# Performance work log

Measured on AMD Instinct MI355X. Metric: run time of the kernel, lower is better.

The kernel has to match this reference:

```python
import jax, jax.numpy as jnp
import numpy as np

B, T, H, N, IN, W, D = 4096, 128, 64, 16, 32, 128, 8


def lipswish(x):
    return 0.909 * jax.nn.silu(x)


def setup_inputs() -> dict:
    key = jax.random.key(0)
    ks = jax.random.split(key, 10)

    def lin(k, i, o):
        kw, kb = jax.random.split(k)
        w = jax.random.normal(kw, (i, o), jnp.float32) / np.sqrt(i).astype(np.float32)
        b = jax.random.normal(kb, (o,), jnp.float32) * 0.01
        return w, b

    init_w0, init_b0 = lin(ks[0], IN, W)
    init_w1, init_b1 = lin(ks[1], W, H)
    drift_w0, drift_b0 = lin(ks[2], H + 1, W)
    drift_w1, drift_b1 = lin(ks[3], W, H)
    diff_w0, diff_b0 = lin(ks[4], H + 1, W)
    diff_w1, diff_b1 = lin(ks[5], W, H * N)
    ro_w, ro_b = lin(ks[6], H, D)
    ts = jnp.arange(T, dtype=jnp.float32)
    init_noise = jax.random.normal(ks[7], (B, IN), jnp.float32)
    # Brownian increments for unit steps: dW ~ N(0, dt) with dt = 1.
    dW = jax.random.normal(ks[8], (B, T - 1, N), jnp.float32)
    return dict(ts=ts, init_noise=init_noise, dW=dW,
                init_w0=init_w0, init_b0=init_b0, init_w1=init_w1, init_b1=init_b1,
                drift_w0=drift_w0, drift_b0=drift_b0, drift_w1=drift_w1, drift_b1=drift_b1,
                diff_w0=diff_w0, diff_b0=diff_b0, diff_w1=diff_w1, diff_b1=diff_b1,
                ro_w=ro_w, ro_b=ro_b)


def reference(ts, init_noise, dW,
              init_w0, init_b0, init_w1, init_b1,
              drift_w0, drift_b0, drift_w1, drift_b1,
              diff_w0, diff_b0, diff_w1, diff_b1,
              ro_w, ro_b):
    # initial MLP: default relu activation, identity final activation
    y0 = jnp.maximum(init_noise @ init_w0 + init_b0, 0.0) @ init_w1 + init_b1  # [B, H]

    def with_t(t, y):
        return jnp.concatenate([jnp.full((y.shape[0], 1), t, y.dtype), y], axis=1)

    def drift(t, y):  # [B, H]
        h = lipswish(with_t(t, y) @ drift_w0 + drift_b0)
        return jnp.tanh(h @ drift_w1 + drift_b1)

    def diffusion(t, y):  # [B, H, N]
        h = lipswish(with_t(t, y) @ diff_w0 + diff_b0)
        g = jnp.tanh(h @ diff_w1 + diff_b1)
        return g.reshape(y.shape[0], H, N)

    f0 = drift(ts[0], y0)
    g0 = diffusion(ts[0], y0)

    def step(carry, inp):
        y, yhat, f, g = carry
        t0, t1, dw = inp  # dw: [B, N]
        dt = t1 - t0
        # ReversibleHeun: yhat1 = 2 y - yhat + (f dt + g dW)
        yhat1 = 2.0 * y - yhat + f * dt + jnp.einsum('bhn,bn->bh', g, dw)
        f1 = drift(t1, yhat1)
        g1 = diffusion(t1, yhat1)
        y1 = y + 0.5 * ((f + f1) * dt + jnp.einsum('bhn,bn->bh', g + g1, dw))
        return (y1, yhat1, f1, g1), y1

    dWs = jnp.swapaxes(dW, 0, 1)  # [T-1, B, N]
    _, ys = jax.lax.scan(step, (y0, y0, f0, g0), (ts[:-1], ts[1:], dWs))
    ys = jnp.concatenate([y0[None], ys], axis=0)  # [T, B, H]
    out = jnp.einsum('tbh,hd->tbd', ys, ro_w) + ro_b
    return jnp.swapaxes(out, 0, 1)  # [B, T, D]
```

## Files before the change

### kernel.cpp

```cpp
#include <hip/hip_runtime.h>

#define NTHREADS 512
#define BB 8
#define SP 68
#define SH 132


struct alignas(16) SMem {
    float dw0[65 * 128];
    float gw0[65 * 128];
    float db0[128];
    float db1[64];
    float gb0[128];
    float ro[512];
    float rob[8];
    float y[BB * SP];
    float yh[BB * SP];
    float f[BB * SP];
    float h[BB * SH];
    float dwn[BB * 16];
};

__device__ __forceinline__ float lipswish_f(float x) {
    const float e = expf(-x);
    const float d = __fadd_rn(1.0f, e);
    const float t = __fmul_rn(0.909f, x);
    return __fdiv_rn(t, d);
}

__global__ __launch_bounds__(NTHREADS, 4)
void sde_kernel(const float* __restrict__ ts, const float* __restrict__ init_noise,
                const float* __restrict__ dWin,
                const float* __restrict__ iw0, const float* __restrict__ ib0,
                const float* __restrict__ iw1, const float* __restrict__ ib1,
                const float* __restrict__ dr_w0, const float* __restrict__ dr_b0,
                const float* __restrict__ dr_w1, const float* __restrict__ dr_b1,
                const float* __restrict__ di_w0, const float* __restrict__ di_b0,
                const float* __restrict__ di_w1, const float* __restrict__ di_b1,
                const float* __restrict__ ro_w, const float* __restrict__ ro_b,
                float* __restrict__ out)
{
    __shared__ SMem sm;
    const int tid  = threadIdx.x;
    const int lane = tid & 63;
    const int wv   = tid >> 6;
    const int b0   = blockIdx.x * BB;

    const int r    = lane & 1;
    const int qn   = (lane >> 1) & 3;
    const int a    = lane >> 3;
    const int c0   = wv * 128 + (lane >> 1) * 4;
    const int rb0  = r * 4;
    const int hh_own = wv * 8 + a;
    const bool owner = ((lane & 6) == 0);
    const int fb = lane >> 3;
    const int fc = wv * 8 + (lane & 7);

    for (int i = tid; i < 65 * 128; i += NTHREADS) {
        sm.dw0[i] = dr_w0[i];
        sm.gw0[i] = di_w0[i];
    }
    if (tid < 128) sm.db0[tid] = dr_b0[tid];
    if (tid < 64)  sm.db1[tid] = dr_b1[tid];
    if (tid < 128) sm.gb0[tid] = di_b0[tid];
    if (tid < 512) sm.ro[tid] = ro_w[tid];
    if (tid < 8) sm.rob[tid] = ro_b[tid];

    float gb1v[4];
    {
        const float4 bv = *(const float4*)&di_b1[c0];
        gb1v[0] = bv.x; gb1v[1] = bv.y; gb1v[2] = bv.z; gb1v[3] = bv.w;
    }

    for (int i = tid; i < BB * 32; i += NTHREADS)
        sm.f[i] = init_noise[(size_t)(b0 + (i >> 5)) * 32 + (i & 31)];
    __syncthreads();

    {
        const int j = tid & 127, bq = tid >> 7;
        float acc[2];
        const float bj = ib0[j];
#pragma unroll
        for (int bi = 0; bi < 2; ++bi) acc[bi] = bj;
        for (int i = 0; i < 32; ++i) {
            const float w = iw0[i * 128 + j];
#pragma unroll
            for (int bi = 0; bi < 2; ++bi)
                acc[bi] = __fmaf_rn(sm.f[(bq * 2 + bi) * 32 + i], w, acc[bi]);
        }
#pragma unroll
        for (int bi = 0; bi < 2; ++bi)
            sm.h[(bq * 2 + bi) * SH + j] = fmaxf(acc[bi], 0.0f);
    }
    __syncthreads();
    {
        const int hh = tid & 63, bg = tid >> 6;
        float acc = ib1[hh];
        for (int k = 0; k < 128; ++k)
            acc = __fmaf_rn(sm.h[bg * SH + k], iw1[k * 64 + hh], acc);
        sm.y[bg * SP + hh]  = acc;
        sm.yh[bg * SP + hh] = acc;
    }
    __syncthreads();

    auto readout = [&](int trow) {
        if (tid < 64) {
            const int b = tid >> 3, d = tid & 7;
            float acc = sm.rob[d];
#pragma unroll
            for (int hh = 0; hh < 64; ++hh)
                acc = __fmaf_rn(sm.y[b * SP + hh], sm.ro[hh * 8 + d], acc);
            out[((size_t)(b0 + b) * 128 + trow) * 8 + d] = acc;
        }
    };
    readout(0);

    float g[4][4];

    auto layer1 = [&](const float* w0s, const float* b0s, float t1f) {
        const int j = tid & 127, bq = tid >> 7;
        float acc[2];
        const float bj = b0s[j];
        const float wt = w0s[j];
#pragma unroll
        for (int bi = 0; bi < 2; ++bi) acc[bi] = __fmaf_rn(t1f, wt, bj);
#pragma unroll 4
        for (int i = 0; i < 64; i += 4) {
            const float w0_ = w0s[(1 + i) * 128 + j];
            const float w1_ = w0s[(2 + i) * 128 + j];
            const float w2_ = w0s[(3 + i) * 128 + j];
            const float w3_ = w0s[(4 + i) * 128 + j];
#pragma unroll
            for (int bi = 0; bi < 2; ++bi) {
                const float4 xv = *(const float4*)&sm.yh[(bq * 2 + bi) * SP + i];
                acc[bi] = __fmaf_rn(xv.x, w0_, acc[bi]);
                acc[bi] = __fmaf_rn(xv.y, w1_, acc[bi]);
                acc[bi] = __fmaf_rn(xv.z, w2_, acc[bi]);
                acc[bi] = __fmaf_rn(xv.w, w3_, acc[bi]);
            }
        }
#pragma unroll
        for (int bi = 0; bi < 2; ++bi)
            sm.h[(bq * 2 + bi) * SH + j] = lipswish_f(acc[bi]);
    };

    auto ein_bfly = [&](const float v[4], int b) -> float {
        float part = 0.0f;
#pragma unroll
        for (int e = 0; e < 4; ++e)
            part = __fmaf_rn(v[e], sm.dwn[b * 16 + qn * 4 + e], part);
        part = __fadd_rn(part, __shfl_xor(part, 2, 64));
        part = __fadd_rn(part, __shfl_xor(part, 4, 64));
        return part;
    };

    auto mlp = [&](float t1f, float dtf, bool upd) {
        layer1(sm.dw0, sm.db0, t1f);
        __syncthreads();
        {
            float acc = sm.db1[fc];
#pragma unroll 4
            for (int k = 0; k < 128; ++k)
                acc = __fmaf_rn(sm.h[fb * SH + k], dr_w1[k * 64 + fc], acc);
            sm.f[fb * SP + fc] = tanhf(acc);
        }
        __syncthreads();
        layer1(sm.gw0, sm.gb0, t1f);
        __syncthreads();
        {
            float acc[4][4];
#pragma unroll
            for (int bi = 0; bi < 4; ++bi)
#pragma unroll
                for (int e = 0; e < 4; ++e) acc[bi][e] = 0.0f;

            float4 wA[4], wB[4], hA[4], hB[4];
#pragma unroll
            for (int t = 0; t < 4; ++t)
                wA[t] = *(const float4*)&di_w1[(size_t)t * 1024 + c0];
#pragma unroll
            for (int bi = 0; bi < 4; ++bi)
                hA[bi] = *(const float4*)&sm.h[(rb0 + bi) * SH];

#pragma unroll 1
            for (int kb = 0; kb < 128; kb += 8) {
                const int k2 = kb + 4;
#pragma unroll
                for (int t = 0; t < 4; ++t)
                    wB[t] = *(const float4*)&di_w1[(size_t)(k2 + t) * 1024 + c0];
#pragma unroll
                for (int bi = 0; bi < 4; ++bi)
                    hB[bi] = *(const float4*)&sm.h[(rb0 + bi) * SH + k2];
#pragma unroll
                for (int bi = 0; bi < 4; ++bi) {
                    acc[bi][0] = __fmaf_rn(hA[bi].x, wA[0].x, acc[bi][0]);
                    acc[bi][1] = __fmaf_rn(hA[bi].x, wA[0].y, acc[bi][1]);
                    acc[bi][2] = __fmaf_rn(hA[bi].x, wA[0].z, acc[bi][2]);
                    acc[bi][3] = __fmaf_rn(hA[bi].x, wA[0].w, acc[bi][3]);
                    acc[bi][0] = __fmaf_rn(hA[bi].y, wA[1].x, acc[bi][0]);
                    acc[bi][1] = __fmaf_rn(hA[bi].y, wA[1].y, acc[bi][1]);
                    acc[bi][2] = __fmaf_rn(hA[bi].y, wA[1].z, acc[bi][2]);
                    acc[bi][3] = __fmaf_rn(hA[bi].y, wA[1].w, acc[bi][3]);
                    acc[bi][0] = __fmaf_rn(hA[bi].z, wA[2].x, acc[bi][0]);
                    acc[bi][1] = __fmaf_rn(hA[bi].z, wA[2].y, acc[bi][1]);
                    acc[bi][2] = __fmaf_rn(hA[bi].z, wA[2].z, acc[bi][2]);
                    acc[bi][3] = __fmaf_rn(hA[bi].z, wA[2].w, acc[bi][3]);
                    acc[bi][0] = __fmaf_rn(hA[bi].w, wA[3].x, acc[bi][0]);
                    acc[bi][1] = __fmaf_rn(hA[bi].w, wA[3].y, acc[bi][1]);
                    acc[bi][2] = __fmaf_rn(hA[bi].w, wA[3].z, acc[bi][2]);
                    acc[bi][3] = __fmaf_rn(hA[bi].w, wA[3].w, acc[bi][3]);
                }
                const int k3 = (kb + 8) & 127;
#pragma unroll
                for (int t = 0; t < 4; ++t)
                    wA[t] = *(const float4*)&di_w1[(size_t)(k3 + t) * 1024 + c0];
#pragma unroll
                for (int bi = 0; bi < 4; ++bi)
                    hA[bi] = *(const float4*)&sm.h[(rb0 + bi) * SH + k3];
#pragma unroll
                for (int bi = 0; bi < 4; ++bi) {
                    acc[bi][0] = __fmaf_rn(hB[bi].x, wB[0].x, acc[bi][0]);
                    acc[bi][1] = __fmaf_rn(hB[bi].x, wB[0].y, acc[bi][1]);
                    acc[bi][2] = __fmaf_rn(hB[bi].x, wB[0].z, acc[bi][2]);
                    acc[bi][3] = __fmaf_rn(hB[bi].x, wB[0].w, acc[bi][3]);
                    acc[bi][0] = __fmaf_rn(hB[bi].y, wB[1].x, acc[bi][0]);
                    acc[bi][1] = __fmaf_rn(hB[bi].y, wB[1].y, acc[bi][1]);
                    acc[bi][2] = __fmaf_rn(hB[bi].y, wB[1].z, acc[bi][2]);
                    acc[bi][3] = __fmaf_rn(hB[bi].y, wB[1].w, acc[bi][3]);
                    acc[bi][0] = __fmaf_rn(hB[bi].z, wB[2].x, acc[bi][0]);
                    acc[bi][1] = __fmaf_rn(hB[bi].z, wB[2].y, acc[bi][1]);
                    acc[bi][2] = __fmaf_rn(hB[bi].z, wB[2].z, acc[bi][2]);
                    acc[bi][3] = __fmaf_rn(hB[bi].z, wB[2].w, acc[bi][3]);
                    acc[bi][0] = __fmaf_rn(hB[bi].w, wB[3].x, acc[bi][0]);
                    acc[bi][1] = __fmaf_rn(hB[bi].w, wB[3].y, acc[bi][1]);
                    acc[bi][2] = __fmaf_rn(hB[bi].w, wB[3].z, acc[bi][2]);
                    acc[bi][3] = __fmaf_rn(hB[bi].w, wB[3].w, acc[bi][3]);
                }
            }

#pragma unroll
            for (int bi = 0; bi < 4; ++bi) {
                const int b = rb0 + bi;
                float gv4[4];
#pragma unroll
                for (int e = 0; e < 4; ++e) {
                    const float gv = tanhf(__fadd_rn(acc[bi][e], gb1v[e]));
                    gv4[e] = gv;
                    g[bi][e] = gv;
                }
                if (upd) {
                    const float ein2 = ein_bfly(gv4, b);
                    if (owner) {
                        const int idx = b * SP + hh_own;
                        const float tot = __fmaf_rn(dtf, sm.f[idx], ein2);
                        sm.y[idx] = __fmaf_rn(0.5f, tot, sm.y[idx]);
                    }
                }
            }
        }
        __syncthreads();
    };

    mlp(ts[0], 0.0f, false);

    for (int s = 0; s < 127; ++s) {
        const float t1f = ts[s + 1];
        const float dtf = __fsub_rn(t1f, ts[s]);

        if (tid < BB * 16)
            sm.dwn[tid] = dWin[((size_t)(b0 + (tid >> 4)) * 127 + s) * 16 + (tid & 15)];
        __syncthreads();

#pragma unroll
        for (int bi = 0; bi < 4; ++bi) {
            const int b = rb0 + bi;
            const float ein1 = ein_bfly(g[bi], b);
            if (owner) {
                const int idx = b * SP + hh_own;
                const float yv  = sm.y[idx];
                const float yhv = sm.yh[idx];
                const float inc = __fmaf_rn(dtf, sm.f[idx], ein1);
                const float a1  = __fmaf_rn(2.0f, yv, -yhv);
                sm.yh[idx] = __fadd_rn(a1, inc);
                sm.y[idx]  = __fmaf_rn(0.5f, inc, yv);
            }
        }
        __syncthreads();

        mlp(t1f, dtf, true);
        readout(s + 1);
    }
}

extern "C" void kernel_launch(void* const* d_in, const int* in_sizes, int n_in,
                              void* d_out, int out_size, void* d_ws, size_t ws_size,
                              hipStream_t stream) {
    (void)in_sizes; (void)n_in; (void)d_ws; (void)ws_size; (void)out_size;
    const float* ts         = (const float*)d_in[0];
    const float* init_noise = (const float*)d_in[1];
    const float* dW         = (const float*)d_in[2];
    const float* iw0        = (const float*)d_in[3];
    const float* ib0        = (const float*)d_in[4];
    const float* iw1        = (const float*)d_in[5];
    const float* ib1        = (const float*)d_in[6];
    const float* dr_w0      = (const float*)d_in[7];
    const float* dr_b0      = (const float*)d_in[8];
    const float* dr_w1      = (const float*)d_in[9];
    const float* dr_b1      = (const float*)d_in[10];
    const float* di_w0      = (const float*)d_in[11];
    const float* di_b0      = (const float*)d_in[12];
    const float* di_w1      = (const float*)d_in[13];
    const float* di_b1      = (const float*)d_in[14];
    const float* ro_w       = (const float*)d_in[15];
    const float* ro_b       = (const float*)d_in[16];
    float* out = (float*)d_out;

    sde_kernel<<<dim3(4096 / BB), dim3(NTHREADS), 0, stream>>>(
        ts, init_noise, dW, iw0, ib0, iw1, ib1,
        dr_w0, dr_b0, dr_w1, dr_b1, di_w0, di_b0, di_w1, di_b1,
        ro_w, ro_b, out);
}
```

Baseline: 3.762 ms.

## Double block threads, drop LDS weight copies, remap diffusion GEMM thread tiling

Raises the block to 1024 threads and remaps the diffusion output-layer work so each thread computes 2 batch rows by 4 columns instead of 4 by 4. The einsum butterfly reduction is changed to match the new lane layout. The first-layer weights for drift and diffusion are now read straight from global memory instead of being staged in LDS, which shrinks shared memory and is meant to allow more resident blocks and higher occupancy. The trade-off is repeated global/L2 reads of those weights at every step, plus half the threads idling in some phases.

Result: slower. 6.048 ms (+60.8%).

```diff
diff --git a/kernel.cpp b/kernel.cpp
--- a/kernel.cpp
+++ b/kernel.cpp
@@ -1,14 +1,12 @@
 #include <hip/hip_runtime.h>
 
-#define NTHREADS 512
+#define NTHREADS 1024
 #define BB 8
 #define SP 68
 #define SH 132
 
 
 struct alignas(16) SMem {
-    float dw0[65 * 128];
-    float gw0[65 * 128];
     float db0[128];
     float db1[64];
     float gb0[128];
@@ -28,7 +26,7 @@
     return __fdiv_rn(t, d);
 }
 
-__global__ __launch_bounds__(NTHREADS, 4)
+__global__ __launch_bounds__(NTHREADS, 8)
 void sde_kernel(const float* __restrict__ ts, const float* __restrict__ init_noise,
                 const float* __restrict__ dWin,
                 const float* __restrict__ iw0, const float* __restrict__ ib0,
@@ -46,20 +44,18 @@
     const int wv   = tid >> 6;
     const int b0   = blockIdx.x * BB;
 
-    const int r    = lane & 1;
-    const int qn   = (lane >> 1) & 3;
-    const int a    = lane >> 3;
-    const int c0   = wv * 128 + (lane >> 1) * 4;
-    const int rb0  = r * 4;
-    const int hh_own = wv * 8 + a;
-    const bool owner = ((lane & 6) == 0);
+    const int cg   = wv & 3;
+    const int rr   = wv >> 2;
+    const int rb0  = rr * 2;
+    const int c0   = cg * 256 + (lane << 2);
+    const int qn   = lane & 3;
+    const int hh_own = cg * 16 + (lane >> 2);
+    const bool owner = (qn == 0);
     const int fb = lane >> 3;
-    const int fc = wv * 8 + (lane & 7);
-
-    for (int i = tid; i < 65 * 128; i += NTHREADS) {
-        sm.dw0[i] = dr_w0[i];
-        sm.gw0[i] = di_w0[i];
-    }
+    const int fc = (wv & 7) * 8 + (lane & 7);
+    const int l1j = tid & 127;
+    const int l1b = tid >> 7;
+
     if (tid < 128) sm.db0[tid] = dr_b0[tid];
     if (tid < 64)  sm.db1[tid] = dr_b1[tid];
     if (tid < 128) sm.gb0[tid] = di_b0[tid];
@@ -72,28 +68,18 @@
         gb1v[0] = bv.x; gb1v[1] = bv.y; gb1v[2] = bv.z; gb1v[3] = bv.w;
     }
 
-    for (int i = tid; i < BB * 32; i += NTHREADS)
-        sm.f[i] = init_noise[(size_t)(b0 + (i >> 5)) * 32 + (i & 31)];
+    if (tid < BB * 32)
+        sm.f[tid] = init_noise[(size_t)(b0 + (tid >> 5)) * 32 + (tid & 31)];
     __syncthreads();
 
     {
-        const int j = tid & 127, bq = tid >> 7;
-        float acc[2];
-        const float bj = ib0[j];
-#pragma unroll
-        for (int bi = 0; bi < 2; ++bi) acc[bi] = bj;
-        for (int i = 0; i < 32; ++i) {
-            const float w = iw0[i * 128 + j];
-#pragma unroll
-            for (int bi = 0; bi < 2; ++bi)
-                acc[bi] = __fmaf_rn(sm.f[(bq * 2 + bi) * 32 + i], w, acc[bi]);
-        }
-#pragma unroll
-        for (int bi = 0; bi < 2; ++bi)
-            sm.h[(bq * 2 + bi) * SH + j] = fmaxf(acc[bi], 0.0f);
+        float acc = ib0[l1j];
+        for (int i = 0; i < 32; ++i)
+            acc = __fmaf_rn(sm.f[l1b * 32 + i], iw0[i * 128 + l1j], acc);
+        sm.h[l1b * SH + l1j] = fmaxf(acc, 0.0f);
     }
     __syncthreads();
-    {
+    if (tid < 512) {
         const int hh = tid & 63, bg = tid >> 6;
         float acc = ib1[hh];
         for (int k = 0; k < 128; ++k)
@@ -115,33 +101,24 @@
     };
     readout(0);
 
-    float g[4][4];
-
-    auto layer1 = [&](const float* w0s, const float* b0s, float t1f) {
-        const int j = tid & 127, bq = tid >> 7;
-        float acc[2];
-        const float bj = b0s[j];
-        const float wt = w0s[j];
-#pragma unroll
-        for (int bi = 0; bi < 2; ++bi) acc[bi] = __fmaf_rn(t1f, wt, bj);
+    float g[2][4];
+
+    auto layer1 = [&](const float* __restrict__ w0g, const float* __restrict__ b0l,
+                      float t1f) {
+        float acc = __fmaf_rn(t1f, w0g[l1j], b0l[l1j]);
 #pragma unroll 4
         for (int i = 0; i < 64; i += 4) {
-            const float w0_ = w0s[(1 + i) * 128 + j];
-            const float w1_ = w0s[(2 + i) * 128 + j];
-            const float w2_ = w0s[(3 + i) * 128 + j];
-            const float w3_ = w0s[(4 + i) * 128 + j];
-#pragma unroll
-            for (int bi = 0; bi < 2; ++bi) {
-                const float4 xv = *(const float4*)&sm.yh[(bq * 2 + bi) * SP + i];
-                acc[bi] = __fmaf_rn(xv.x, w0_, acc[bi]);
-                acc[bi] = __fmaf_rn(xv.y, w1_, acc[bi]);
-                acc[bi] = __fmaf_rn(xv.z, w2_, acc[bi]);
-                acc[bi] = __fmaf_rn(xv.w, w3_, acc[bi]);
-            }
-        }
-#pragma unroll
-        for (int bi = 0; bi < 2; ++bi)
-            sm.h[(bq * 2 + bi) * SH + j] = lipswish_f(acc[bi]);
+            const float w0_ = w0g[(1 + i) * 128 + l1j];
+            const float w1_ = w0g[(2 + i) * 128 + l1j];
+            const float w2_ = w0g[(3 + i) * 128 + l1j];
+            const float w3_ = w0g[(4 + i) * 128 + l1j];
+            const float4 xv = *(const float4*)&sm.yh[l1b * SP + i];
+            acc = __fmaf_rn(xv.x, w0_, acc);
+            acc = __fmaf_rn(xv.y, w1_, acc);
+            acc = __fmaf_rn(xv.z, w2_, acc);
+            acc = __fmaf_rn(xv.w, w3_, acc);
+        }
+        sm.h[l1b * SH + l1j] = lipswish_f(acc);
     };
 
     auto ein_bfly = [&](const float v[4], int b) -> float {
@@ -149,15 +126,15 @@
 #pragma unroll
         for (int e = 0; e < 4; ++e)
             part = __fmaf_rn(v[e], sm.dwn[b * 16 + qn * 4 + e], part);
+        part = __fadd_rn(part, __shfl_xor(part, 1, 64));
         part = __fadd_rn(part, __shfl_xor(part, 2, 64));
-        part = __fadd_rn(part, __shfl_xor(part, 4, 64));
         return part;
     };
 
     auto mlp = [&](float t1f, float dtf, bool upd) {
-        layer1(sm.dw0, sm.db0, t1f);
-        __syncthreads();
-        {
+        layer1(dr_w0, sm.db0, t1f);
+        __syncthreads();
+        if (tid < 512) {
             float acc = sm.db1[fc];
 #pragma unroll 4
             for (int k = 0; k < 128; ++k)
@@ -165,81 +142,45 @@
             sm.f[fb * SP + fc] = tanhf(acc);
         }
         __syncthreads();
-        layer1(sm.gw0, sm.gb0, t1f);
+        layer1(di_w0, sm.gb0, t1f);
         __syncthreads();
         {
-            float acc[4][4];
-#pragma unroll
-            for (int bi = 0; bi < 4; ++bi)
+            float acc[2][4];
+#pragma unroll
+            for (int bi = 0; bi < 2; ++bi)
 #pragma unroll
                 for (int e = 0; e < 4; ++e) acc[bi][e] = 0.0f;
 
-            float4 wA[4], wB[4], hA[4], hB[4];
-#pragma unroll
-            for (int t = 0; t < 4; ++t)
-                wA[t] = *(const float4*)&di_w1[(size_t)t * 1024 + c0];
-#pragma unroll
-            for (int bi = 0; bi < 4; ++bi)
-                hA[bi] = *(const float4*)&sm.h[(rb0 + bi) * SH];
-
-#pragma unroll 1
-            for (int kb = 0; kb < 128; kb += 8) {
-                const int k2 = kb + 4;
-#pragma unroll
-                for (int t = 0; t < 4; ++t)
-                    wB[t] = *(const float4*)&di_w1[(size_t)(k2 + t) * 1024 + c0];
-#pragma unroll
-                for (int bi = 0; bi < 4; ++bi)
-                    hB[bi] = *(const float4*)&sm.h[(rb0 + bi) * SH + k2];
-#pragma unroll
-                for (int bi = 0; bi < 4; ++bi) {
-                    acc[bi][0] = __fmaf_rn(hA[bi].x, wA[0].x, acc[bi][0]);
-                    acc[bi][1] = __fmaf_rn(hA[bi].x, wA[0].y, acc[bi][1]);
-                    acc[bi][2] = __fmaf_rn(hA[bi].x, wA[0].z, acc[bi][2]);
-                    acc[bi][3] = __fmaf_rn(hA[bi].x, wA[0].w, acc[bi][3]);
-                    acc[bi][0] = __fmaf_rn(hA[bi].y, wA[1].x, acc[bi][0]);
-                    acc[bi][1] = __fmaf_rn(hA[bi].y, wA[1].y, acc[bi][1]);
-                    acc[bi][2] = __fmaf_rn(hA[bi].y, wA[1].z, acc[bi][2]);
-                    acc[bi][3] = __fmaf_rn(hA[bi].y, wA[1].w, acc[bi][3]);
-                    acc[bi][0] = __fmaf_rn(hA[bi].z, wA[2].x, acc[bi][0]);
-                    acc[bi][1] = __fmaf_rn(hA[bi].z, wA[2].y, acc[bi][1]);
-                    acc[bi][2] = __fmaf_rn(hA[bi].z, wA[2].z, acc[bi][2]);
-                    acc[bi][3] = __fmaf_rn(hA[bi].z, wA[2].w, acc[bi][3]);
-                    acc[bi][0] = __fmaf_rn(hA[bi].w, wA[3].x, acc[bi][0]);
-                    acc[bi][1] = __fmaf_rn(hA[bi].w, wA[3].y, acc[bi][1]);
-                    acc[bi][2] = __fmaf_rn(hA[bi].w, wA[3].z, acc[bi][2]);
-                    acc[bi][3] = __fmaf_rn(hA[bi].w, wA[3].w, acc[bi][3]);
-                }
-                const int k3 = (kb + 8) & 127;
-#pragma unroll
-                for (int t = 0; t < 4; ++t)
-                    wA[t] = *(const float4*)&di_w1[(size_t)(k3 + t) * 1024 + c0];
-#pragma unroll
-                for (int bi = 0; bi < 4; ++bi)
-                    hA[bi] = *(const float4*)&sm.h[(rb0 + bi) * SH + k3];
-#pragma unroll
-                for (int bi = 0; bi < 4; ++bi) {
-                    acc[bi][0] = __fmaf_rn(hB[bi].x, wB[0].x, acc[bi][0]);
-                    acc[bi][1] = __fmaf_rn(hB[bi].x, wB[0].y, acc[bi][1]);
-                    acc[bi][2] = __fmaf_rn(hB[bi].x, wB[0].z, acc[bi][2]);
-                    acc[bi][3] = __fmaf_rn(hB[bi].x, wB[0].w, acc[bi][3]);
-                    acc[bi][0] = __fmaf_rn(hB[bi].y, wB[1].x, acc[bi][0]);
-                    acc[bi][1] = __fmaf_rn(hB[bi].y, wB[1].y, acc[bi][1]);
-                    acc[bi][2] = __fmaf_rn(hB[bi].y, wB[1].z, acc[bi][2]);
-                    acc[bi][3] = __fmaf_rn(hB[bi].y, wB[1].w, acc[bi][3]);
-                    acc[bi][0] = __fmaf_rn(hB[bi].z, wB[2].x, acc[bi][0]);
-                    acc[bi][1] = __fmaf_rn(hB[bi].z, wB[2].y, acc[bi][1]);
-                    acc[bi][2] = __fmaf_rn(hB[bi].z, wB[2].z, acc[bi][2]);
-                    acc[bi][3] = __fmaf_rn(hB[bi].z, wB[2].w, acc[bi][3]);
-                    acc[bi][0] = __fmaf_rn(hB[bi].w, wB[3].x, acc[bi][0]);
-                    acc[bi][1] = __fmaf_rn(hB[bi].w, wB[3].y, acc[bi][1]);
-                    acc[bi][2] = __fmaf_rn(hB[bi].w, wB[3].z, acc[bi][2]);
-                    acc[bi][3] = __fmaf_rn(hB[bi].w, wB[3].w, acc[bi][3]);
+#pragma unroll 2
+            for (int kb = 0; kb < 128; kb += 4) {
+                const float4 w0 = *(const float4*)&di_w1[(size_t)(kb + 0) * 1024 + c0];
+                const float4 w1 = *(const float4*)&di_w1[(size_t)(kb + 1) * 1024 + c0];
+                const float4 w2 = *(const float4*)&di_w1[(size_t)(kb + 2) * 1024 + c0];
+                const float4 w3 = *(const float4*)&di_w1[(size_t)(kb + 3) * 1024 + c0];
+#pragma unroll
+                for (int bi = 0; bi < 2; ++bi) {
+                    const float4 hv = *(const float4*)&sm.h[(rb0 + bi) * SH + kb];
+                    acc[bi][0] = __fmaf_rn(hv.x, w0.x, acc[bi][0]);
+                    acc[bi][1] = __fmaf_rn(hv.x, w0.y, acc[bi][1]);
+                    acc[bi][2] = __fmaf_rn(hv.x, w0.z, acc[bi][2]);
+                    acc[bi][3] = __fmaf_rn(hv.x, w0.w, acc[bi][3]);
+                    acc[bi][0] = __fmaf_rn(hv.y, w1.x, acc[bi][0]);
+                    acc[bi][1] = __fmaf_rn(hv.y, w1.y, acc[bi][1]);
+                    acc[bi][2] = __fmaf_rn(hv.y, w1.z, acc[bi][2]);
+                    acc[bi][3] = __fmaf_rn(hv.y, w1.w, acc[bi][3]);
+                    acc[bi][0] = __fmaf_rn(hv.z, w2.x, acc[bi][0]);
+                    acc[bi][1] = __fmaf_rn(hv.z, w2.y, acc[bi][1]);
+                    acc[bi][2] = __fmaf_rn(hv.z, w2.z, acc[bi][2]);
+                    acc[bi][3] = __fmaf_rn(hv.z, w2.w, acc[bi][3]);
+                    acc[bi][0] = __fmaf_rn(hv.w, w3.x, acc[bi][0]);
+                    acc[bi][1] = __fmaf_rn(hv.w, w3.y, acc[bi][1]);
+                    acc[bi][2] = __fmaf_rn(hv.w, w3.z, acc[bi][2]);
+                    acc[bi][3] = __fmaf_rn(hv.w, w3.w, acc[bi][3]);
                 }
             }
 
 #pragma unroll
-            for (int bi = 0; bi < 4; ++bi) {
+            for (int bi = 0; bi < 2; ++bi) {
                 const int b = rb0 + bi;
                 float gv4[4];
 #pragma unroll
@@ -272,7 +213,7 @@
         __syncthreads();
 
 #pragma unroll
-        for (int bi = 0; bi < 4; ++bi) {
+        for (int bi = 0; bi < 2; ++bi) {
             const int b = rb0 + bi;
             const float ein1 = ein_bfly(g[bi], b);
             if (owner) {
```

## Halve block to 4 batch rows and read first-layer weights from global

Applied to the files above, without the earlier changes.

Reduces the block from 512 threads and 8 batch rows to 256 threads and 4 rows, and remaps the diffusion second-layer ownership so each thread covers all 4 rows with a 2-step butterfly reduction. It also drops the two 65x128 first-layer weight tables from LDS, reading them straight from global memory (L1/L2 cached). The aim is to shrink shared memory per block so more blocks fit per CU and the serial step chain overlaps better. In exchange, global weight traffic per batch row doubles and the per-block setup staging is gone.

Result: slower. 4.271 ms (+13.5%).

```diff
diff --git a/kernel.cpp b/kernel.cpp
--- a/kernel.cpp
+++ b/kernel.cpp
@@ -1,14 +1,12 @@
 #include <hip/hip_runtime.h>
 
-#define NTHREADS 512
-#define BB 8
+#define NTHREADS 256
+#define BB 4
 #define SP 68
 #define SH 132
 
 
 struct alignas(16) SMem {
-    float dw0[65 * 128];
-    float gw0[65 * 128];
     float db0[128];
     float db1[64];
     float gb0[128];
@@ -46,24 +44,17 @@
     const int wv   = tid >> 6;
     const int b0   = blockIdx.x * BB;
 
-    const int r    = lane & 1;
-    const int qn   = (lane >> 1) & 3;
-    const int a    = lane >> 3;
-    const int c0   = wv * 128 + (lane >> 1) * 4;
-    const int rb0  = r * 4;
-    const int hh_own = wv * 8 + a;
-    const bool owner = ((lane & 6) == 0);
-    const int fb = lane >> 3;
-    const int fc = wv * 8 + (lane & 7);
-
-    for (int i = tid; i < 65 * 128; i += NTHREADS) {
-        sm.dw0[i] = dr_w0[i];
-        sm.gw0[i] = di_w0[i];
-    }
+    const int c0   = wv * 256 + (lane << 2);
+    const int qn   = lane & 3;
+    const int hh_own = wv * 16 + (lane >> 2);
+    const bool owner = (qn == 0);
+    const int fb = lane >> 4;
+    const int fc = wv * 16 + (lane & 15);
+
     if (tid < 128) sm.db0[tid] = dr_b0[tid];
     if (tid < 64)  sm.db1[tid] = dr_b1[tid];
     if (tid < 128) sm.gb0[tid] = di_b0[tid];
-    if (tid < 512) sm.ro[tid] = ro_w[tid];
+    for (int i = tid; i < 512; i += NTHREADS) sm.ro[i] = ro_w[i];
     if (tid < 8) sm.rob[tid] = ro_b[tid];
 
     float gb1v[4];
@@ -72,8 +63,8 @@
         gb1v[0] = bv.x; gb1v[1] = bv.y; gb1v[2] = bv.z; gb1v[3] = bv.w;
     }
 
-    for (int i = tid; i < BB * 32; i += NTHREADS)
-        sm.f[i] = init_noise[(size_t)(b0 + (i >> 5)) * 32 + (i & 31)];
+    if (tid < BB * 32)
+        sm.f[tid] = init_noise[(size_t)(b0 + (tid >> 5)) * 32 + (tid & 31)];
     __syncthreads();
 
     {
@@ -104,7 +95,7 @@
     __syncthreads();
 
     auto readout = [&](int trow) {
-        if (tid < 64) {
+        if (tid < 32) {
             const int b = tid >> 3, d = tid & 7;
             float acc = sm.rob[d];
 #pragma unroll
@@ -117,10 +108,11 @@
 
     float g[4][4];
 
-    auto layer1 = [&](const float* w0s, const float* b0s, float t1f) {
+    auto layer1 = [&](const float* __restrict__ w0s, const float* __restrict__ b0l,
+                      float t1f) {
         const int j = tid & 127, bq = tid >> 7;
         float acc[2];
-        const float bj = b0s[j];
+        const float bj = b0l[j];
         const float wt = w0s[j];
 #pragma unroll
         for (int bi = 0; bi < 2; ++bi) acc[bi] = __fmaf_rn(t1f, wt, bj);
@@ -149,13 +141,13 @@
 #pragma unroll
         for (int e = 0; e < 4; ++e)
             part = __fmaf_rn(v[e], sm.dwn[b * 16 + qn * 4 + e], part);
+        part = __fadd_rn(part, __shfl_xor(part, 1, 64));
         part = __fadd_rn(part, __shfl_xor(part, 2, 64));
-        part = __fadd_rn(part, __shfl_xor(part, 4, 64));
         return part;
     };
 
     auto mlp = [&](float t1f, float dtf, bool upd) {
-        layer1(sm.dw0, sm.db0, t1f);
+        layer1(dr_w0, sm.db0, t1f);
         __syncthreads();
         {
             float acc = sm.db1[fc];
@@ -165,7 +157,7 @@
             sm.f[fb * SP + fc] = tanhf(acc);
         }
         __syncthreads();
-        layer1(sm.gw0, sm.gb0, t1f);
+        layer1(di_w0, sm.gb0, t1f);
         __syncthreads();
         {
             float acc[4][4];
@@ -180,7 +172,7 @@
                 wA[t] = *(const float4*)&di_w1[(size_t)t * 1024 + c0];
 #pragma unroll
             for (int bi = 0; bi < 4; ++bi)
-                hA[bi] = *(const float4*)&sm.h[(rb0 + bi) * SH];
+                hA[bi] = *(const float4*)&sm.h[bi * SH];
 
 #pragma unroll 1
             for (int kb = 0; kb < 128; kb += 8) {
@@ -190,7 +182,7 @@
                     wB[t] = *(const float4*)&di_w1[(size_t)(k2 + t) * 1024 + c0];
 #pragma unroll
                 for (int bi = 0; bi < 4; ++bi)
-                    hB[bi] = *(const float4*)&sm.h[(rb0 + bi) * SH + k2];
+                    hB[bi] = *(const float4*)&sm.h[bi * SH + k2];
 #pragma unroll
                 for (int bi = 0; bi < 4; ++bi) {
                     acc[bi][0] = __fmaf_rn(hA[bi].x, wA[0].x, acc[bi][0]);
@@ -216,7 +208,7 @@
                     wA[t] = *(const float4*)&di_w1[(size_t)(k3 + t) * 1024 + c0];
 #pragma unroll
                 for (int bi = 0; bi < 4; ++bi)
-                    hA[bi] = *(const float4*)&sm.h[(rb0 + bi) * SH + k3];
+                    hA[bi] = *(const float4*)&sm.h[bi * SH + k3];
 #pragma unroll
                 for (int bi = 0; bi < 4; ++bi) {
                     acc[bi][0] = __fmaf_rn(hB[bi].x, wB[0].x, acc[bi][0]);
@@ -240,7 +232,6 @@
 
 #pragma unroll
             for (int bi = 0; bi < 4; ++bi) {
-                const int b = rb0 + bi;
                 float gv4[4];
 #pragma unroll
                 for (int e = 0; e < 4; ++e) {
@@ -249,9 +240,9 @@
                     g[bi][e] = gv;
                 }
                 if (upd) {
-                    const float ein2 = ein_bfly(gv4, b);
+                    const float ein2 = ein_bfly(gv4, bi);
                     if (owner) {
-                        const int idx = b * SP + hh_own;
+                        const int idx = bi * SP + hh_own;
                         const float tot = __fmaf_rn(dtf, sm.f[idx], ein2);
                         sm.y[idx] = __fmaf_rn(0.5f, tot, sm.y[idx]);
                     }
@@ -273,10 +264,9 @@
 
 #pragma unroll
         for (int bi = 0; bi < 4; ++bi) {
-            const int b = rb0 + bi;
-            const float ein1 = ein_bfly(g[bi], b);
+            const float ein1 = ein_bfly(g[bi], bi);
             if (owner) {
-                const int idx = b * SP + hh_own;
+                const int idx = bi * SP + hh_own;
                 const float yv  = sm.y[idx];
                 const float yhv = sm.yh[idx];
                 const float inc = __fmaf_rn(dtf, sm.f[idx], ein1);
```
